# Kernel optimization log

Measured on AMD Instinct MI355X. Metric: run time of the kernel, lower is better.

Reference implementation:

```python
import jax, jax.numpy as jnp
import numpy as np

EPS = 1e-8
VOX_WIDTH = 1.0
CURV_THRESH = 0.5


def _build_kernels():
    """Nine 3x3x3 central finite-difference stencils, pre-divided by vox_width / vox_width^2."""
    def zk():
        return np.zeros((3, 3, 3), np.float32)
    ks = {}
    # first derivatives (central difference), denominator vox_width
    for name, ax in (('ddx', 0), ('ddy', 1), ('ddz', 2)):
        k = zk(); i = [1, 1, 1]
        i[ax] = 0; k[tuple(i)] = -0.5
        i[ax] = 2; k[tuple(i)] = 0.5
        ks[name] = k / VOX_WIDTH
    # pure second derivatives, denominator vox_width^2
    for name, ax in (('d2dx2', 0), ('d2dy2', 1), ('d2dz2', 2)):
        k = zk(); i = [1, 1, 1]
        i[ax] = 0; k[tuple(i)] = 1.0
        i[ax] = 1; k[tuple(i)] = -2.0
        i[ax] = 2; k[tuple(i)] = 1.0
        ks[name] = k / VOX_WIDTH ** 2
    # mixed second derivatives, denominator vox_width^2
    for name, (a, b) in (('d2dxdy', (0, 1)), ('d2dxdz', (0, 2)), ('d2dydz', (1, 2))):
        k = zk()
        for sa, sb, v in ((0, 0, 0.25), (0, 2, -0.25), (2, 0, -0.25), (2, 2, 0.25)):
            i = [1, 1, 1]; i[a] = sa; i[b] = sb; k[tuple(i)] = v
        ks[name] = k / VOX_WIDTH ** 2
    order = ['ddx', 'ddy', 'ddz', 'd2dx2', 'd2dy2', 'd2dz2', 'd2dxdy', 'd2dxdz', 'd2dydz']
    return np.stack([ks[n] for n in order])[:, None]  # [9, 1, 3, 3, 3]


_KERNELS = jnp.asarray(_build_kernels())


def setup_inputs() -> dict:
    key = jax.random.key(0)
    phi = jax.random.normal(key, (2, 1, 192, 192, 192), dtype=jnp.float32)
    return {"phi": phi}


def reference(phi):
    # all nine stencils as one valid 3D conv: [N, 9, D-2, H-2, W-2]
    g = jax.lax.conv_general_dilated(
        phi, _KERNELS, window_strides=(1, 1, 1), padding='VALID',
        dimension_numbers=('NCDHW', 'OIDHW', 'NCDHW'))
    gx, gy, gz, hxx, hyy, hzz, hxy, hxz, hyz = (g[:, i:i + 1] for i in range(9))

    mag = jnp.sqrt(gx * gx + gy * gy + gz * gz + EPS)
    mag3 = mag ** 3

    # mean curvature: sum_{i!=j} g_i^2 H_jj - 2 sum_{i<j} g_i g_j H_ij, over |grad|^3
    cross = gx * gy * hxy + gx * gz * hxz + gy * gz * hyz
    mean_c = (gx * gx * (hyy + hzz) + gy * gy * (hxx + hzz) + gz * gz * (hxx + hyy)
              - 2.0 * cross) / (mag3 + EPS)

    # gaussian curvature: laplacian/|grad| - (g^T H g)/|grad|^3
    lap = (hxx + hyy + hzz) / (mag + EPS)
    quad = (gx * gx * hxx + gy * gy * hyy + gz * gz * hzz + 2.0 * cross) / (mag3 + EPS)
    gauss = lap - quad

    k1 = mean_c + jnp.sqrt(jnp.abs(mean_c ** 2 - gauss) + EPS)
    pen = jax.nn.relu((k1 / (CURV_THRESH + EPS)) ** 2 - 1.0)

    # zero crossings of phi over 3x3x3 neighborhoods (valid -> matches conv output shape)
    mn = jax.lax.reduce_window(phi, jnp.inf, jax.lax.min, (1, 1, 3, 3, 3), (1, 1, 1, 1, 1), 'VALID')
    mx = jax.lax.reduce_window(phi, -jnp.inf, jax.lax.max, (1, 1, 3, 3, 3), (1, 1, 1, 1, 1), 'VALID')
    phi_zero = jax.lax.stop_gradient((mn * mx < 0).astype(phi.dtype))

    return jnp.sum(phi_zero * pen) / (jnp.sum(phi_zero) + EPS)
```

## Files before the change

### kernel.cpp

```cpp
#include <hip/hip_runtime.h>


constexpr int DIM  = 192;
constexpr int ODIM = 190;
constexpr int TX = 32, TY = 32, CZ = 6;
constexpr int NTX = 6, NTY = 6, NTZ = 32;
constexpr int HX = 34, HY = 34;
constexpr int LX = 36;
constexpr int NELEM = HX * HY;
constexpr int NBLOCKS = 2 * NTZ * NTY * NTX;

struct Slice {
    float v[3][6];
    float mn[6], mx[6];
};

__global__ __launch_bounds__(256, 4) void curv_main(const float* __restrict__ phi,
                                                    double* __restrict__ acc,
                                                    int use_partials) {
    __shared__ __align__(16) float tile[3][HY][LX];

    int bx = blockIdx.x;
    const int tx = bx % NTX; bx /= NTX;
    const int ty = bx % NTY; bx /= NTY;
    const int tz = bx % NTZ; bx /= NTZ;
    const int n  = bx;

    const int xbase = tx * TX, ybase = ty * TY, zbase = tz * CZ;
    const int tid = threadIdx.x;
    const float* pn = phi + (long long)n * DIM * DIM * DIM;

    int goff[5], loff[5];
#pragma unroll
    for (int it = 0; it < 5; ++it) {
        int idx = tid + it * 256; if (idx > NELEM - 1) idx = NELEM - 1;
        int ly = idx / HX, lx = idx - ly * HX;
        int iy = ybase + ly; if (iy > DIM - 1) iy = DIM - 1;
        int ix = xbase + lx; if (ix > DIM - 1) ix = DIM - 1;
        goff[it] = iy * DIM + ix;
        loff[it] = ly * LX + lx;
    }

    float pf[5];
    auto pref = [&](int g) {
        int gz = zbase + g; if (gz > DIM - 1) gz = DIM - 1;
        const float* src = pn + gz * DIM * DIM;
#pragma unroll
        for (int it = 0; it < 5; ++it) pf[it] = src[goff[it]];
    };
    float* tf = &tile[0][0][0];
    auto commit = [&](int slot) {
        float* t = tf + slot * (HY * LX);
#pragma unroll
        for (int it = 0; it < 5; ++it) t[loff[it]] = pf[it];
    };

    const int row = tid >> 3;
    const int x0  = (tid & 7) * 4;

    auto read_slice = [&](int slot, Slice& s) {
#pragma unroll
        for (int dy = 0; dy < 3; ++dy) {
            const float* rp = &tile[slot][row + dy][x0];
            const float4 a = *(const float4*)rp;
            const float2 b = *(const float2*)(rp + 4);
            s.v[dy][0] = a.x; s.v[dy][1] = a.y; s.v[dy][2] = a.z;
            s.v[dy][3] = a.w; s.v[dy][4] = b.x; s.v[dy][5] = b.y;
        }
#pragma unroll
        for (int c = 0; c < 6; ++c) {
            s.mn[c] = fminf(fminf(s.v[0][c], s.v[1][c]), s.v[2][c]);
            s.mx[c] = fmaxf(fmaxf(s.v[0][c], s.v[1][c]), s.v[2][c]);
        }
    };

    double sp = 0.0, sc = 0.0;
    const float EPSF = 1e-8f;
    const int oy = ybase + row;
    const bool vy = (oy < ODIM);

    auto compute = [&](const Slice& s0, const Slice& s1, const Slice& s2, int zo) {
        const int oz = zbase + zo;
        if (oz >= ODIM) return;

        float colmn[6], colmx[6];
#pragma unroll
        for (int c = 0; c < 6; ++c) {
            colmn[c] = fminf(fminf(s0.mn[c], s1.mn[c]), s2.mn[c]);
            colmx[c] = fmaxf(fmaxf(s0.mx[c], s1.mx[c]), s2.mx[c]);
        }

        float fsp = 0.0f, fsc = 0.0f;
#pragma unroll
        for (int j = 0; j < 4; ++j) {
            const int ox = xbase + x0 + j;
            const bool valid = vy && (ox < ODIM);

            float gx = 0.5f * (s2.v[1][j + 1] - s0.v[1][j + 1]);
            float gy = 0.5f * (s1.v[2][j + 1] - s1.v[0][j + 1]);
            float gz = 0.5f * (s1.v[1][j + 2] - s1.v[1][j]);

            float c2  = 2.0f * s1.v[1][j + 1];
            float hxx = s0.v[1][j + 1] - c2 + s2.v[1][j + 1];
            float hyy = s1.v[0][j + 1] - c2 + s1.v[2][j + 1];
            float hzz = s1.v[1][j] - c2 + s1.v[1][j + 2];

            float hxy = 0.25f * (s0.v[0][j + 1] - s0.v[2][j + 1]
                               - s2.v[0][j + 1] + s2.v[2][j + 1]);
            float hxz = 0.25f * (s0.v[1][j] - s0.v[1][j + 2]
                               - s2.v[1][j] + s2.v[1][j + 2]);
            float hyz = 0.25f * (s1.v[0][j] - s1.v[0][j + 2]
                               - s1.v[2][j] + s1.v[2][j + 2]);

            float gx2 = gx * gx, gy2 = gy * gy, gz2 = gz * gz;
            float mag  = sqrtf(gx2 + gy2 + gz2 + EPSF);
            float mag3 = mag * mag * mag;

            float cross = gx * gy * hxy + gx * gz * hxz + gy * gz * hyz;
            float inv_mag3 = __builtin_amdgcn_rcpf(mag3 + EPSF);
            float inv_mag  = __builtin_amdgcn_rcpf(mag  + EPSF);

            float mean_c = (gx2 * (hyy + hzz) + gy2 * (hxx + hzz) +
                            gz2 * (hxx + hyy) - 2.0f * cross) * inv_mag3;
            float lap   = (hxx + hyy + hzz) * inv_mag;
            float quad  = (gx2 * hxx + gy2 * hyy + gz2 * hzz + 2.0f * cross) * inv_mag3;
            float gauss = lap - quad;

            float k1  = mean_c + sqrtf(fabsf(mean_c * mean_c - gauss) + EPSF);
            float t   = k1 * 2.0f;
            float pen = fmaxf(t * t - 1.0f, 0.0f);

            float mn = fminf(fminf(colmn[j], colmn[j + 1]), colmn[j + 2]);
            float mx = fmaxf(fmaxf(colmx[j], colmx[j + 1]), colmx[j + 2]);

            if (valid && (mn * mx < 0.0f)) {
                fsp += pen;
                fsc += 1.0f;
            }
        }
        sp += (double)fsp;
        sc += (double)fsc;
    };

    Slice s0, s1, s2;

    pref(0); commit(0);
    pref(1); commit(1);
    pref(2);
    __syncthreads();
    read_slice(0, s0);
    read_slice(1, s1);

    commit(2); pref(3); __syncthreads(); read_slice(2, s2); compute(s0, s1, s2, 0);
    commit(0); pref(4); __syncthreads(); read_slice(0, s0); compute(s1, s2, s0, 1);
    commit(1); pref(5); __syncthreads(); read_slice(1, s1); compute(s2, s0, s1, 2);
    commit(2); pref(6); __syncthreads(); read_slice(2, s2); compute(s0, s1, s2, 3);
    commit(0); pref(7); __syncthreads(); read_slice(0, s0); compute(s1, s2, s0, 4);
    commit(1);          __syncthreads(); read_slice(1, s1); compute(s2, s0, s1, 5);

#pragma unroll
    for (int off = 32; off > 0; off >>= 1) {
        sp += __shfl_down(sp, off, 64);
        sc += __shfl_down(sc, off, 64);
    }

    __shared__ double lsp[4], lsc[4];
    const int wave = tid >> 6, lane = tid & 63;
    if (lane == 0) { lsp[wave] = sp; lsc[wave] = sc; }
    __syncthreads();
    if (tid == 0) {
        double tp = lsp[0] + lsp[1] + lsp[2] + lsp[3];
        double tc = lsc[0] + lsc[1] + lsc[2] + lsc[3];
        if (use_partials) {
            acc[2 * blockIdx.x]     = tp;
            acc[2 * blockIdx.x + 1] = tc;
        } else {
            atomicAdd(&acc[0], tp);
            atomicAdd(&acc[1], tc);
        }
    }
}

__global__ __launch_bounds__(256) void curv_reduce(const double* __restrict__ part,
                                                   int nblocks, int use_partials,
                                                   float* __restrict__ out) {
    double sp = 0.0, sc = 0.0;
    if (use_partials) {
        for (int i = threadIdx.x; i < nblocks; i += 256) {
            sp += part[2 * i];
            sc += part[2 * i + 1];
        }
    } else if (threadIdx.x == 0) {
        sp = part[0]; sc = part[1];
    }
#pragma unroll
    for (int off = 32; off > 0; off >>= 1) {
        sp += __shfl_down(sp, off, 64);
        sc += __shfl_down(sc, off, 64);
    }
    __shared__ double lsp[4], lsc[4];
    const int wave = threadIdx.x >> 6, lane = threadIdx.x & 63;
    if (lane == 0) { lsp[wave] = sp; lsc[wave] = sc; }
    __syncthreads();
    if (threadIdx.x == 0) {
        double tp = lsp[0] + lsp[1] + lsp[2] + lsp[3];
        double tc = lsc[0] + lsc[1] + lsc[2] + lsc[3];
        out[0] = (float)(tp / (tc + 1e-8));
    }
}

extern "C" void kernel_launch(void* const* d_in, const int* in_sizes, int n_in,
                              void* d_out, int out_size, void* d_ws, size_t ws_size,
                              hipStream_t stream) {
    const float* phi = (const float*)d_in[0];
    float* out = (float*)d_out;
    double* acc = (double*)d_ws;

    const int use_partials = (ws_size >= (size_t)(2 * NBLOCKS) * sizeof(double)) ? 1 : 0;
    if (!use_partials) {
        hipMemsetAsync(d_ws, 0, 2 * sizeof(double), stream);
    }

    curv_main<<<NBLOCKS, 256, 0, stream>>>(phi, acc, use_partials);
    curv_reduce<<<1, 256, 0, stream>>>(acc, NBLOCKS, use_partials, out);
}
```

Before: 118.7 us.

## Pack stencil math into float2 vectors and deepen z-chunk per block

Rewrites the per-voxel curvature math on two-wide float vectors so the compiler can emit packed FP32 instructions (v_pk_fma/mul), pairing columns j and j+2. Increases the z outputs per block from 6 to 7, which cuts the block count and the halo reloads per output. It also drops redundant LDS stores on the fifth halo pass, and folds the min/max into the slice read. Packed math may add register pressure and repacking moves, and the larger chunk leaves fewer blocks to spread across the GPU.

```diff
diff --git a/kernel.cpp b/kernel.cpp
--- a/kernel.cpp
+++ b/kernel.cpp
@@ -1,17 +1,19 @@
 #include <hip/hip_runtime.h>
 
+
+typedef float v2f __attribute__((ext_vector_type(2)));
 
 constexpr int DIM  = 192;
 constexpr int ODIM = 190;
-constexpr int TX = 32, TY = 32, CZ = 6;
-constexpr int NTX = 6, NTY = 6, NTZ = 32;
+constexpr int TX = 32, TY = 32, CZ = 7;
+constexpr int NTX = 6, NTY = 6, NTZ = 28;
 constexpr int HX = 34, HY = 34;
 constexpr int LX = 36;
 constexpr int NELEM = HX * HY;
 constexpr int NBLOCKS = 2 * NTZ * NTY * NTX;
 
 struct Slice {
-    float v[3][6];
+    v2f   q[3][4];
     float mn[6], mx[6];
 };
 
@@ -40,6 +42,7 @@
         goff[it] = iy * DIM + ix;
         loff[it] = ly * LX + lx;
     }
+    const bool st5 = (tid + 1024 < NELEM);
 
     float pf[5];
     auto pref = [&](int g) {
@@ -52,7 +55,8 @@
     auto commit = [&](int slot) {
         float* t = tf + slot * (HY * LX);
 #pragma unroll
-        for (int it = 0; it < 5; ++it) t[loff[it]] = pf[it];
+        for (int it = 0; it < 4; ++it) t[loff[it]] = pf[it];
+        if (st5) t[loff[4]] = pf[4];
     };
 
     const int row = tid >> 3;
@@ -64,20 +68,34 @@
             const float* rp = &tile[slot][row + dy][x0];
             const float4 a = *(const float4*)rp;
             const float2 b = *(const float2*)(rp + 4);
-            s.v[dy][0] = a.x; s.v[dy][1] = a.y; s.v[dy][2] = a.z;
-            s.v[dy][3] = a.w; s.v[dy][4] = b.x; s.v[dy][5] = b.y;
-        }
-#pragma unroll
-        for (int c = 0; c < 6; ++c) {
-            s.mn[c] = fminf(fminf(s.v[0][c], s.v[1][c]), s.v[2][c]);
-            s.mx[c] = fmaxf(fmaxf(s.v[0][c], s.v[1][c]), s.v[2][c]);
+            s.q[dy][0] = (v2f){a.x, a.z};
+            s.q[dy][1] = (v2f){a.y, a.w};
+            s.q[dy][2] = (v2f){a.z, b.x};
+            s.q[dy][3] = (v2f){a.w, b.y};
+            if (dy == 0) {
+                s.mn[0] = a.x; s.mn[1] = a.y; s.mn[2] = a.z;
+                s.mn[3] = a.w; s.mn[4] = b.x; s.mn[5] = b.y;
+                s.mx[0] = a.x; s.mx[1] = a.y; s.mx[2] = a.z;
+                s.mx[3] = a.w; s.mx[4] = b.x; s.mx[5] = b.y;
+            } else {
+                s.mn[0] = fminf(s.mn[0], a.x); s.mx[0] = fmaxf(s.mx[0], a.x);
+                s.mn[1] = fminf(s.mn[1], a.y); s.mx[1] = fmaxf(s.mx[1], a.y);
+                s.mn[2] = fminf(s.mn[2], a.z); s.mx[2] = fmaxf(s.mx[2], a.z);
+                s.mn[3] = fminf(s.mn[3], a.w); s.mx[3] = fmaxf(s.mx[3], a.w);
+                s.mn[4] = fminf(s.mn[4], b.x); s.mx[4] = fmaxf(s.mx[4], b.x);
+                s.mn[5] = fminf(s.mn[5], b.y); s.mx[5] = fmaxf(s.mx[5], b.y);
+            }
         }
     };
 
     double sp = 0.0, sc = 0.0;
     const float EPSF = 1e-8f;
     const int oy = ybase + row;
-    const bool vy = (oy < ODIM);
+
+    bool vmask[4];
+#pragma unroll
+    for (int j = 0; j < 4; ++j)
+        vmask[j] = (oy < ODIM) && (xbase + x0 + j < ODIM);
 
     auto compute = [&](const Slice& s0, const Slice& s1, const Slice& s2, int zo) {
         const int oz = zbase + zo;
@@ -92,50 +110,57 @@
 
         float fsp = 0.0f, fsc = 0.0f;
 #pragma unroll
-        for (int j = 0; j < 4; ++j) {
-            const int ox = xbase + x0 + j;
-            const bool valid = vy && (ox < ODIM);
-
-            float gx = 0.5f * (s2.v[1][j + 1] - s0.v[1][j + 1]);
-            float gy = 0.5f * (s1.v[2][j + 1] - s1.v[0][j + 1]);
-            float gz = 0.5f * (s1.v[1][j + 2] - s1.v[1][j]);
-
-            float c2  = 2.0f * s1.v[1][j + 1];
-            float hxx = s0.v[1][j + 1] - c2 + s2.v[1][j + 1];
-            float hyy = s1.v[0][j + 1] - c2 + s1.v[2][j + 1];
-            float hzz = s1.v[1][j] - c2 + s1.v[1][j + 2];
-
-            float hxy = 0.25f * (s0.v[0][j + 1] - s0.v[2][j + 1]
-                               - s2.v[0][j + 1] + s2.v[2][j + 1]);
-            float hxz = 0.25f * (s0.v[1][j] - s0.v[1][j + 2]
-                               - s2.v[1][j] + s2.v[1][j + 2]);
-            float hyz = 0.25f * (s1.v[0][j] - s1.v[0][j + 2]
-                               - s1.v[2][j] + s1.v[2][j + 2]);
-
-            float gx2 = gx * gx, gy2 = gy * gy, gz2 = gz * gz;
-            float mag  = sqrtf(gx2 + gy2 + gz2 + EPSF);
-            float mag3 = mag * mag * mag;
-
-            float cross = gx * gy * hxy + gx * gz * hxz + gy * gz * hyz;
-            float inv_mag3 = __builtin_amdgcn_rcpf(mag3 + EPSF);
-            float inv_mag  = __builtin_amdgcn_rcpf(mag  + EPSF);
-
-            float mean_c = (gx2 * (hyy + hzz) + gy2 * (hxx + hzz) +
-                            gz2 * (hxx + hyy) - 2.0f * cross) * inv_mag3;
-            float lap   = (hxx + hyy + hzz) * inv_mag;
-            float quad  = (gx2 * hxx + gy2 * hyy + gz2 * hzz + 2.0f * cross) * inv_mag3;
-            float gauss = lap - quad;
-
-            float k1  = mean_c + sqrtf(fabsf(mean_c * mean_c - gauss) + EPSF);
-            float t   = k1 * 2.0f;
-            float pen = fmaxf(t * t - 1.0f, 0.0f);
-
-            float mn = fminf(fminf(colmn[j], colmn[j + 1]), colmn[j + 2]);
-            float mx = fmaxf(fmaxf(colmx[j], colmx[j + 1]), colmx[j + 2]);
-
-            if (valid && (mn * mx < 0.0f)) {
-                fsp += pen;
-                fsc += 1.0f;
+        for (int p = 0; p < 2; ++p) {
+            v2f gx = 0.5f * (s2.q[1][p + 1] - s0.q[1][p + 1]);
+            v2f gy = 0.5f * (s1.q[2][p + 1] - s1.q[0][p + 1]);
+            v2f gz = 0.5f * (s1.q[1][p + 2] - s1.q[1][p]);
+
+            v2f c2  = 2.0f * s1.q[1][p + 1];
+            v2f hxx = s0.q[1][p + 1] - c2 + s2.q[1][p + 1];
+            v2f hyy = s1.q[0][p + 1] - c2 + s1.q[2][p + 1];
+            v2f hzz = s1.q[1][p] - c2 + s1.q[1][p + 2];
+
+            v2f hxy = 0.25f * (s0.q[0][p + 1] - s0.q[2][p + 1]
+                             - s2.q[0][p + 1] + s2.q[2][p + 1]);
+            v2f hxz = 0.25f * (s0.q[1][p] - s0.q[1][p + 2]
+                             - s2.q[1][p] + s2.q[1][p + 2]);
+            v2f hyz = 0.25f * (s1.q[0][p] - s1.q[0][p + 2]
+                             - s1.q[2][p] + s1.q[2][p + 2]);
+
+            v2f gx2 = gx * gx, gy2 = gy * gy, gz2 = gz * gz;
+            v2f mag2 = gx2 + gy2 + gz2 + EPSF;
+            v2f mag  = (v2f){ sqrtf(mag2.x), sqrtf(mag2.y) };
+            v2f mag3 = mag2 * mag;
+
+            v2f cross = gx * gy * hxy + gx * gz * hxz + gy * gz * hyz;
+            v2f inv3 = (v2f){ __builtin_amdgcn_rcpf(mag3.x + EPSF),
+                              __builtin_amdgcn_rcpf(mag3.y + EPSF) };
+            v2f inv1 = (v2f){ __builtin_amdgcn_rcpf(mag.x + EPSF),
+                              __builtin_amdgcn_rcpf(mag.y + EPSF) };
+
+            v2f mean_c = (gx2 * (hyy + hzz) + gy2 * (hxx + hzz) +
+                          gz2 * (hxx + hyy) - 2.0f * cross) * inv3;
+            v2f lap   = (hxx + hyy + hzz) * inv1;
+            v2f quad  = (gx2 * hxx + gy2 * hyy + gz2 * hzz + 2.0f * cross) * inv3;
+            v2f gauss = lap - quad;
+
+            v2f disc = mean_c * mean_c - gauss;
+            v2f sq = (v2f){ sqrtf(fabsf(disc.x) + EPSF),
+                            sqrtf(fabsf(disc.y) + EPSF) };
+            v2f k1 = mean_c + sq;
+            v2f t  = 2.0f * k1;
+            v2f pen2 = t * t - 1.0f;
+
+#pragma unroll
+            for (int e = 0; e < 2; ++e) {
+                const int j = p + 2 * e;
+                float pen = fmaxf(e ? pen2.y : pen2.x, 0.0f);
+                float mn = fminf(fminf(colmn[j], colmn[j + 1]), colmn[j + 2]);
+                float mx = fmaxf(fmaxf(colmx[j], colmx[j + 1]), colmx[j + 2]);
+                if (vmask[j] && (mn * mx < 0.0f)) {
+                    fsp += pen;
+                    fsc += 1.0f;
+                }
             }
         }
         sp += (double)fsp;
@@ -156,7 +181,8 @@
     commit(1); pref(5); __syncthreads(); read_slice(1, s1); compute(s2, s0, s1, 2);
     commit(2); pref(6); __syncthreads(); read_slice(2, s2); compute(s0, s1, s2, 3);
     commit(0); pref(7); __syncthreads(); read_slice(0, s0); compute(s1, s2, s0, 4);
-    commit(1);          __syncthreads(); read_slice(1, s1); compute(s2, s0, s1, 5);
+    commit(1); pref(8); __syncthreads(); read_slice(1, s1); compute(s2, s0, s1, 5);
+    commit(2);          __syncthreads(); read_slice(2, s2); compute(s0, s1, s2, 6);
 
 #pragma unroll
     for (int off = 32; off > 0; off >>= 1) {
```

Result: slower. 165.8 us (+39.7%).
